# Optimization experiments

Hardware: AMD Instinct MI355X
Metric: run time of the kernel (lower is better)

Reference implementation:

```python
import jax, jax.numpy as jnp
import numpy as np

WIN_SIZE = 8          # img_size // win_num = 56 // 7
HEADS = 12
EMB = 384
HEAD_DIM = EMB // HEADS   # 32
ATT = WIN_SIZE ** 2       # 64 tokens per window
SCALE = HEAD_DIM ** -0.5
BATCH, NWIN = 32, 49


def _rel_index(ws: int) -> np.ndarray:
    # Faithful port of WinMSA.getIndex: relative-position index table (ws^2, ws^2)
    ys, xs = np.meshgrid(np.arange(ws), np.arange(ws), indexing='ij')
    coords = np.stack([ys, xs], axis=-1).reshape(-1, 2)            # (ws^2, 2)
    diff = coords[None, :, :] - coords[:, None, :] + (ws - 1)      # (ws^2, ws^2, 2)
    return diff[:, :, 0] * (2 * ws - 1) + diff[:, :, 1]            # values in [0, (2ws-1)^2)


def setup_inputs() -> dict:
    key = jax.random.key(0)
    k_x, k_qkv, k_pb, k_o = jax.random.split(key, 4)
    X = jax.random.normal(k_x, (BATCH, NWIN, ATT, EMB), dtype=jnp.float32)
    # qkv Linear (no bias): stored as (in, 3*in) so x @ W_qkv matches torch x @ W.T
    W_qkv = jax.random.normal(k_qkv, (EMB, 3 * EMB), dtype=jnp.float32) * 0.02
    # positional bias table, literal module shape (heads, 2*att-1, 2*att-1)
    pos_bias = jax.random.normal(k_pb, (HEADS, 2 * ATT - 1, 2 * ATT - 1), dtype=jnp.float32) * 0.02
    W_o = jax.random.normal(k_o, (EMB, EMB), dtype=jnp.float32) * 0.02
    b_o = jnp.zeros((EMB,), dtype=jnp.float32)
    relp = jnp.asarray(_rel_index(WIN_SIZE), dtype=jnp.int32)       # (ATT, ATT)
    return {"X": X, "W_qkv": W_qkv, "pos_bias": pos_bias, "W_o": W_o, "b_o": b_o, "relp": relp}


def reference(X, W_qkv, pos_bias, W_o, b_o, relp):
    B, Wn, S, E = X.shape
    # fused QKV projection
    qkv = (X @ W_qkv).reshape(B, Wn, S, 3, HEADS, HEAD_DIM)
    qkv = jnp.transpose(qkv, (3, 0, 1, 4, 2, 5))                    # (3, B, Wn, H, S, Dh)
    q, k, v = qkv[0], qkv[1], qkv[2]
    # gathered relative position bias: (H, S, S)
    bias = pos_bias.reshape(HEADS, -1)[:, relp]
    attn = jnp.einsum('bwhqd,bwhkd->bwhqk', q, k) * SCALE + bias[None, None]
    proba = jax.nn.softmax(attn, axis=-1)                           # dropout: eval mode (identity)
    out = jnp.einsum('bwhqk,bwhkd->bwhqd', proba, v)                # (B, Wn, H, S, Dh)
    out = jnp.transpose(out, (0, 1, 3, 2, 4)).reshape(B, Wn, S, E)
    return out @ W_o + b_o
```

## Files before the change

### kernel.cpp

```cpp
#include <hip/hip_runtime.h>
#include <hip/hip_bf16.h>

typedef float f32x4 __attribute__((ext_vector_type(4)));
typedef short s16x8 __attribute__((ext_vector_type(8)));

#define MFMA16(A,B,C) __builtin_amdgcn_mfma_f32_16x16x32_bf16((A),(B),(C),0,0,0)

__device__ __forceinline__ short f2bf(float f) {
  return (short)__bfloat16_as_ushort(__float2bfloat16(f));
}

__device__ __forceinline__ void gload_lds16(const void* g, void* l) {
  __builtin_amdgcn_global_load_lds(
      (const __attribute__((address_space(1))) unsigned*)g,
      (__attribute__((address_space(3))) unsigned*)l, 16, 0, 0);
}

__global__ __launch_bounds__(256) void prep_kernel(
    const float* __restrict__ Wqkv, const float* __restrict__ Wo,
    const float* __restrict__ posb, const int* __restrict__ relp,
    short* __restrict__ WqkvT, short* __restrict__ WoT, float* __restrict__ biasF)
{
  int i = blockIdx.x * 256 + threadIdx.x;
  if (i < 1152 * 384) {
    int n = i / 384, k = i % 384;
    WqkvT[i] = f2bf(Wqkv[k * 1152 + n]);
  } else if (i < 1152 * 384 + 384 * 384) {
    int j = i - 1152 * 384;
    int n = j / 384, k = j % 384;
    WoT[j] = f2bf(Wo[k * 384 + n]);
  } else {
    int j = i - (1152 * 384 + 384 * 384);
    int h = j >> 12, qk = j & 4095;
    biasF[j] = posb[h * 16129 + relp[qk]];
  }
}

__global__ __launch_bounds__(256) void xcvt_kernel(
    const float* __restrict__ X, short* __restrict__ Xbf)
{
  const int n8 = 4816896;
  for (int i = blockIdx.x * 256 + threadIdx.x; i < n8; i += gridDim.x * 256) {
    float4 a = *(const float4*)(X + (size_t)i * 8);
    float4 b = *(const float4*)(X + (size_t)i * 8 + 4);
    s16x8 p;
    p[0] = f2bf(a.x); p[1] = f2bf(a.y); p[2] = f2bf(a.z); p[3] = f2bf(a.w);
    p[4] = f2bf(b.x); p[5] = f2bf(b.y); p[6] = f2bf(b.z); p[7] = f2bf(b.w);
    *(s16x8*)(Xbf + (size_t)i * 8) = p;
  }
}

__global__ __launch_bounds__(256) void qkv_attn(
    const short* __restrict__ Xbf, const short* __restrict__ WqkvT,
    const float* __restrict__ biasF, short* __restrict__ AO)
{
  __shared__ short lds[40960];
  const int bid = blockIdx.x;
  const int wg = (bid & 7) * 588 + (bid >> 3);
  const int hg = wg % 6, mt = wg / 6;
  const int t = threadIdx.x;
  const int wv = t >> 6, l = t & 63, lr = l & 15, lg = l >> 4;
  const int wm = wv >> 1, wn = wv & 1;

  f32x4 acc[6][4];
#pragma unroll
  for (int fn = 0; fn < 6; ++fn)
#pragma unroll
    for (int fm = 0; fm < 4; ++fm) acc[fn][fm] = (f32x4)0.0f;

  const int cgs = (l & 7) ^ (l >> 3);
  const short* AbT = Xbf + (size_t)(mt * 128 + wv * 32 + (l >> 3)) * 384 + cgs * 8;
  const short* BbT[6];
#pragma unroll
  for (int j = 0; j < 6; ++j) {
    const int n0 = wv * 48 + j * 8 + (l >> 3);
    const int hl = n0 / 96, rem = n0 % 96;
    const int p = rem >> 5, d = rem & 31;
    BbT[j] = WqkvT + (size_t)(p * 384 + hg * 64 + hl * 32 + d) * 384 + cgs * 8;
  }

#define STAGE(KS, SEL) do {                                                  \
  _Pragma("unroll")                                                          \
  for (int i_ = 0; i_ < 4; ++i_)                                             \
    gload_lds16(AbT + i_ * 3072 + (KS) * 64,                                 \
                lds + (SEL) * 8192 + (wv * 4 + i_) * 512);                   \
  _Pragma("unroll")                                                          \
  for (int j_ = 0; j_ < 6; ++j_)                                             \
    gload_lds16(BbT[j_] + (KS) * 64,                                         \
                lds + 16384 + (SEL) * 12288 + (wv * 6 + j_) * 512);          \
  } while (0)

#define COMPUTE(SEL) do {                                                    \
  const short* Acur_ = lds + (SEL) * 8192;                                   \
  const short* Bcur_ = lds + 16384 + (SEL) * 12288;                          \
  _Pragma("unroll")                                                          \
  for (int kk = 0; kk < 2; ++kk) {                                           \
    s16x8 af[4], bq[6];                                                      \
    _Pragma("unroll")                                                        \
    for (int f = 0; f < 4; ++f) {                                            \
      const int arow = wm * 64 + f * 16 + lr;                                \
      const int ac = (kk * 4 + lg) ^ (arow & 7);                             \
      af[f] = *(const s16x8*)(Acur_ + arow * 64 + ac * 8);                   \
    }                                                                        \
    _Pragma("unroll")                                                        \
    for (int fn = 0; fn < 6; ++fn) {                                         \
      const int brow = wn * 96 + fn * 16 + lr;                               \
      const int bc = (kk * 4 + lg) ^ (brow & 7);                             \
      bq[fn] = *(const s16x8*)(Bcur_ + brow * 64 + bc * 8);                  \
    }                                                                        \
    _Pragma("unroll")                                                        \
    for (int fn = 0; fn < 6; ++fn)                                           \
      _Pragma("unroll")                                                      \
      for (int fm = 0; fm < 4; ++fm)                                         \
        acc[fn][fm] = MFMA16(bq[fn], af[fm], acc[fn][fm]);        \
  } } while (0)

#define ITER(T, WN) do {                                                     \
  asm volatile("s_waitcnt vmcnt(" #WN ")" ::: "memory");                     \
  __builtin_amdgcn_s_barrier();                                              \
  COMPUTE((T) & 1);                                                          \
  asm volatile("s_waitcnt lgkmcnt(0)" ::: "memory");          \
  __builtin_amdgcn_s_barrier();                                              \
  if ((T) + 2 < 6) STAGE((T) + 2, (T) & 1);                                  \
  } while (0)

  STAGE(0, 0);
  STAGE(1, 1);
  ITER(0, 10); ITER(1, 10); ITER(2, 10); ITER(3, 10); ITER(4, 10); ITER(5, 0);
#undef ITER
#undef COMPUTE
#undef STAGE


  const int w = mt * 2 + wm, h = hg * 2 + wn;
  short* Vts = lds + wv * 4992;
  short* Os  = Vts + 2432;

#pragma unroll
  for (int fv = 0; fv < 2; ++fv)
#pragma unroll
    for (int fm = 0; fm < 4; ++fm)
#pragma unroll
      for (int r = 0; r < 4; ++r)
        Vts[(fv * 16 + lg * 4 + r) * 76 + fm * 16 + lr] =
            f2bf(acc[4 + fv][fm][r]);

  s16x8 ka[4], qb[4];
#pragma unroll
  for (int f = 0; f < 4; ++f) {
    s16x8 tk, tq;
#pragma unroll
    for (int j = 0; j < 8; ++j) {
      tk[j] = f2bf(acc[2 + (j >> 2)][f][j & 3]);
      tq[j] = f2bf(acc[0 + (j >> 2)][f][j & 3]);
    }
    ka[f] = tk; qb[f] = tq;
  }

  f32x4 st[4][4];
#pragma unroll
  for (int fk = 0; fk < 4; ++fk)
#pragma unroll
    for (int fq = 0; fq < 4; ++fq)
      st[fk][fq] = MFMA16(ka[fk], qb[fq], (f32x4)0.0f);

  const float* bh = biasF + h * 4096;
#pragma unroll
  for (int fq = 0; fq < 4; ++fq) {
    const int q = fq * 16 + lr;
    float4 bv[4];
#pragma unroll
    for (int fk = 0; fk < 4; ++fk)
      bv[fk] = *(const float4*)(bh + q * 64 + fk * 16 + lg * 4);
    float mx = -3.0e38f;
#pragma unroll
    for (int fk = 0; fk < 4; ++fk)
#pragma unroll
      for (int r = 0; r < 4; ++r) {
        float v = st[fk][fq][r] * 0.17677669529663687f + ((const float*)&bv[fk])[r];
        st[fk][fq][r] = v;
        mx = fmaxf(mx, v);
      }
    mx = fmaxf(mx, __shfl_xor(mx, 16));
    mx = fmaxf(mx, __shfl_xor(mx, 32));
    float sm = 0.0f;
#pragma unroll
    for (int fk = 0; fk < 4; ++fk)
#pragma unroll
      for (int r = 0; r < 4; ++r) {
        float e = __expf(st[fk][fq][r] - mx);
        st[fk][fq][r] = e;
        sm += e;
      }
    sm += __shfl_xor(sm, 16);
    sm += __shfl_xor(sm, 32);
    const float inv = 1.0f / sm;
#pragma unroll
    for (int fk = 0; fk < 4; ++fk)
#pragma unroll
      for (int r = 0; r < 4; ++r) st[fk][fq][r] *= inv;
  }

  s16x8 va[2][2];
#pragma unroll
  for (int fd = 0; fd < 2; ++fd)
#pragma unroll
    for (int kb = 0; kb < 2; ++kb) {
      short4 v0 = *(const short4*)(Vts + (fd * 16 + lr) * 76 + kb * 32 + lg * 4);
      short4 v1 = *(const short4*)(Vts + (fd * 16 + lr) * 76 + kb * 32 + 16 + lg * 4);
      s16x8 tv;
      tv[0] = v0.x; tv[1] = v0.y; tv[2] = v0.z; tv[3] = v0.w;
      tv[4] = v1.x; tv[5] = v1.y; tv[6] = v1.z; tv[7] = v1.w;
      va[fd][kb] = tv;
    }
  f32x4 ot[2][4];
#pragma unroll
  for (int fd = 0; fd < 2; ++fd)
#pragma unroll
    for (int fq = 0; fq < 4; ++fq) ot[fd][fq] = (f32x4)0.0f;
#pragma unroll
  for (int kb = 0; kb < 2; ++kb)
#pragma unroll
    for (int fq = 0; fq < 4; ++fq) {
      s16x8 pb;
#pragma unroll
      for (int j = 0; j < 8; ++j)
        pb[j] = f2bf(st[2 * kb + (j >> 2)][fq][j & 3]);
#pragma unroll
      for (int fd = 0; fd < 2; ++fd)
        ot[fd][fq] = MFMA16(va[fd][kb], pb, ot[fd][fq]);
    }

#pragma unroll
  for (int fd = 0; fd < 2; ++fd)
#pragma unroll
    for (int fq = 0; fq < 4; ++fq)
#pragma unroll
      for (int r = 0; r < 4; ++r)
        Os[(fq * 16 + lr) * 40 + fd * 16 + lg * 4 + r] = f2bf(ot[fd][fq][r]);
  short* dst = AO + ((size_t)w * 64 + l) * 384 + h * 32;
  int4 o0 = *(const int4*)(Os + l * 40);
  int4 o1 = *(const int4*)(Os + l * 40 + 8);
  int4 o2 = *(const int4*)(Os + l * 40 + 16);
  int4 o3 = *(const int4*)(Os + l * 40 + 24);
  *(int4*)(dst)      = o0;
  *(int4*)(dst + 8)  = o1;
  *(int4*)(dst + 16) = o2;
  *(int4*)(dst + 24) = o3;
}

__global__ __launch_bounds__(256) void proj_kernel(
    const short* __restrict__ AO, const short* __restrict__ WoT,
    const float* __restrict__ bo, float* __restrict__ out)
{
  __shared__ short lds[32768];
  const int bid = blockIdx.x;
  const int wg = (bid & 7) * 294 + (bid >> 3);
  const int nt = wg % 3, mt = wg / 3;
  const int t = threadIdx.x;
  const int wv = t >> 6, l = t & 63, lr = l & 15, lg = l >> 4;
  const int wm = wv >> 1, wn = wv & 1;

  f32x4 acc[4][4];
#pragma unroll
  for (int fm = 0; fm < 4; ++fm)
#pragma unroll
    for (int fn = 0; fn < 4; ++fn) acc[fm][fn] = (f32x4)0.0f;

  const int srow = wv * 32 + (l >> 3);
  const int cg = (l & 7) ^ (srow & 7);
  const short* Ab = AO  + (size_t)(mt * 128 + srow) * 384 + cg * 8;
  const short* Bb = WoT + (size_t)(nt * 128 + srow) * 384 + cg * 8;

#define STAGE(KS, SEL) do {                                                  \
  _Pragma("unroll")                                                          \
  for (int i_ = 0; i_ < 4; ++i_) {                                           \
    gload_lds16(Ab + i_ * 3072 + (KS) * 64,                                  \
                lds + (SEL) * 16384 + (wv * 4 + i_) * 512);                  \
    gload_lds16(Bb + i_ * 3072 + (KS) * 64,                                  \
                lds + (SEL) * 16384 + 8192 + (wv * 4 + i_) * 512);           \
  } } while (0)

#define COMPUTE(SEL) do {                                                    \
  const short* Acur_ = lds + (SEL) * 16384;                                  \
  const short* Bcur_ = Acur_ + 8192;                                         \
  _Pragma("unroll")                                                          \
  for (int kk = 0; kk < 2; ++kk) {                                           \
    s16x8 af[4], bf[4];                                                      \
    _Pragma("unroll")                                                        \
    for (int f = 0; f < 4; ++f) {                                            \
      const int arow = wm * 64 + f * 16 + lr;                                \
      const int ac = (kk * 4 + lg) ^ (arow & 7);                             \
      af[f] = *(const s16x8*)(Acur_ + arow * 64 + ac * 8);                   \
      const int brow = wn * 64 + f * 16 + lr;                                \
      const int bc = (kk * 4 + lg) ^ (brow & 7);                             \
      bf[f] = *(const s16x8*)(Bcur_ + brow * 64 + bc * 8);                   \
    }                                                                        \
    _Pragma("unroll")                                                        \
    for (int fm = 0; fm < 4; ++fm)                                           \
      _Pragma("unroll")                                                      \
      for (int fn = 0; fn < 4; ++fn)                                         \
        acc[fm][fn] = MFMA16(af[fm], bf[fn], acc[fm][fn]);                   \
  } } while (0)

#define ITER(T, WN) do {                                                     \
  asm volatile("s_waitcnt vmcnt(" #WN ")" ::: "memory");                     \
  __builtin_amdgcn_s_barrier();                                              \
  COMPUTE((T) & 1);                                                          \
  asm volatile("s_waitcnt lgkmcnt(0)" ::: "memory");          \
  __builtin_amdgcn_s_barrier();                                              \
  if ((T) + 2 < 6) STAGE((T) + 2, (T) & 1);                                  \
  } while (0)

  STAGE(0, 0);
  STAGE(1, 1);
  ITER(0, 8); ITER(1, 8); ITER(2, 8); ITER(3, 8); ITER(4, 8); ITER(5, 0);
#undef ITER
#undef COMPUTE
#undef STAGE

#pragma unroll
  for (int fn = 0; fn < 4; ++fn) {
    const int n = nt * 128 + wn * 64 + fn * 16 + lr;
    const float bias = bo[n];
#pragma unroll
    for (int fm = 0; fm < 4; ++fm) {
      const int m0 = mt * 128 + wm * 64 + fm * 16 + lg * 4;
#pragma unroll
      for (int r = 0; r < 4; ++r)
        out[(size_t)(m0 + r) * 384 + n] = acc[fm][fn][r] + bias;
    }
  }
}

extern "C" void kernel_launch(void* const* d_in, const int* in_sizes, int n_in,
                              void* d_out, int out_size, void* d_ws, size_t ws_size,
                              hipStream_t stream)
{
  const float* X    = (const float*)d_in[0];
  const float* Wqkv = (const float*)d_in[1];
  const float* posb = (const float*)d_in[2];
  const float* Wo   = (const float*)d_in[3];
  const float* bo   = (const float*)d_in[4];
  const int*   relp = (const int*)d_in[5];
  float* out = (float*)d_out;

  char* ws = (char*)d_ws;
  short* WqkvT = (short*)(ws);
  short* WoT   = (short*)(ws + 884736);
  float* biasF = (float*)(ws + 1179648);
  short* Xbf   = (short*)(ws + 1376256);
  short* AO    = (short*)(ws + 78446592);

  prep_kernel<<<2496, 256, 0, stream>>>(Wqkv, Wo, posb, relp, WqkvT, WoT, biasF);
  xcvt_kernel<<<2048, 256, 0, stream>>>(X, Xbf);
  qkv_attn<<<4704, 256, 0, stream>>>(Xbf, WqkvT, biasF, AO);
  proj_kernel<<<2352, 256, 0, stream>>>(AO, WoT, bo, out);
}
```

Before: 232.6 us.

## Load QKV weight fragments directly into registers and shrink LDS for occupancy

The weight (B) operand of the QKV GEMM is no longer staged through LDS. Each wave now reads its MFMA fragments straight from global memory into registers inside the compute loop. The LDS allocation shrinks to just the X tiles and the attention scratch, and launch bounds request 4 blocks per CU so more workgroups can be resident. The trade-off is that the weight loads now sit in the vmcnt-ordered queue behind the prefetched A loads, so some global latency may be exposed instead of hidden by the double-buffered pipeline.

```diff
diff --git a/kernel.cpp b/kernel.cpp
--- a/kernel.cpp
+++ b/kernel.cpp
@@ -50,11 +50,11 @@
   }
 }
 
-__global__ __launch_bounds__(256) void qkv_attn(
+__global__ __launch_bounds__(256, 4) void qkv_attn(
     const short* __restrict__ Xbf, const short* __restrict__ WqkvT,
     const float* __restrict__ biasF, short* __restrict__ AO)
 {
-  __shared__ short lds[40960];
+  __shared__ short lds[19968];
   const int bid = blockIdx.x;
   const int wg = (bid & 7) * 588 + (bid >> 3);
   const int hg = wg % 6, mt = wg / 6;
@@ -70,32 +70,27 @@
 
   const int cgs = (l & 7) ^ (l >> 3);
   const short* AbT = Xbf + (size_t)(mt * 128 + wv * 32 + (l >> 3)) * 384 + cgs * 8;
-  const short* BbT[6];
-#pragma unroll
-  for (int j = 0; j < 6; ++j) {
-    const int n0 = wv * 48 + j * 8 + (l >> 3);
-    const int hl = n0 / 96, rem = n0 % 96;
-    const int p = rem >> 5, d = rem & 31;
-    BbT[j] = WqkvT + (size_t)(p * 384 + hg * 64 + hl * 32 + d) * 384 + cgs * 8;
-  }
+  const short* Bb[6];
+#pragma unroll
+  for (int fn = 0; fn < 6; ++fn)
+    Bb[fn] = WqkvT + (size_t)((fn >> 1) * 384 + hg * 64 + wn * 32
+                              + (fn & 1) * 16 + lr) * 384 + lg * 8;
 
 #define STAGE(KS, SEL) do {                                                  \
   _Pragma("unroll")                                                          \
   for (int i_ = 0; i_ < 4; ++i_)                                             \
     gload_lds16(AbT + i_ * 3072 + (KS) * 64,                                 \
                 lds + (SEL) * 8192 + (wv * 4 + i_) * 512);                   \
-  _Pragma("unroll")                                                          \
-  for (int j_ = 0; j_ < 6; ++j_)                                             \
-    gload_lds16(BbT[j_] + (KS) * 64,                                         \
-                lds + 16384 + (SEL) * 12288 + (wv * 6 + j_) * 512);          \
   } while (0)
 
-#define COMPUTE(SEL) do {                                                    \
-  const short* Acur_ = lds + (SEL) * 8192;                                   \
-  const short* Bcur_ = lds + 16384 + (SEL) * 12288;                          \
+#define COMPUTE(T) do {                                                      \
+  const short* Acur_ = lds + ((T) & 1) * 8192;                               \
   _Pragma("unroll")                                                          \
   for (int kk = 0; kk < 2; ++kk) {                                           \
     s16x8 af[4], bq[6];                                                      \
+    _Pragma("unroll")                                                        \
+    for (int fn = 0; fn < 6; ++fn)                                           \
+      bq[fn] = *(const s16x8*)(Bb[fn] + (T) * 64 + kk * 32);                 \
     _Pragma("unroll")                                                        \
     for (int f = 0; f < 4; ++f) {                                            \
       const int arow = wm * 64 + f * 16 + lr;                                \
@@ -103,12 +98,6 @@
       af[f] = *(const s16x8*)(Acur_ + arow * 64 + ac * 8);                   \
     }                                                                        \
     _Pragma("unroll")                                                        \
-    for (int fn = 0; fn < 6; ++fn) {                                         \
-      const int brow = wn * 96 + fn * 16 + lr;                               \
-      const int bc = (kk * 4 + lg) ^ (brow & 7);                             \
-      bq[fn] = *(const s16x8*)(Bcur_ + brow * 64 + bc * 8);                  \
-    }                                                                        \
-    _Pragma("unroll")                                                        \
     for (int fn = 0; fn < 6; ++fn)                                           \
       _Pragma("unroll")                                                      \
       for (int fm = 0; fm < 4; ++fm)                                         \
@@ -118,7 +107,7 @@
 #define ITER(T, WN) do {                                                     \
   asm volatile("s_waitcnt vmcnt(" #WN ")" ::: "memory");                     \
   __builtin_amdgcn_s_barrier();                                              \
-  COMPUTE((T) & 1);                                                          \
+  COMPUTE(T);                                                                \
   asm volatile("s_waitcnt lgkmcnt(0)" ::: "memory");          \
   __builtin_amdgcn_s_barrier();                                              \
   if ((T) + 2 < 6) STAGE((T) + 2, (T) & 1);                                  \
@@ -126,7 +115,7 @@
 
   STAGE(0, 0);
   STAGE(1, 1);
-  ITER(0, 10); ITER(1, 10); ITER(2, 10); ITER(3, 10); ITER(4, 10); ITER(5, 0);
+  ITER(0, 4); ITER(1, 4); ITER(2, 4); ITER(3, 4); ITER(4, 4); ITER(5, 0);
 #undef ITER
 #undef COMPUTE
 #undef STAGE
```

Result: slower. 863.0 us (+271.0%).

## Fuse X fp32-to-bf16 conversion into QKV attention kernel A-tile loads

Applied to the files above, without the earlier changes.

Removes the standalone conversion kernel and instead loads fp32 X tiles into registers inside the QKV/attention kernel, converting to bf16 and writing to LDS with software pipelining alongside the async weight loads. This eliminates a full write and reread of the bf16 copy of X and one kernel launch. In exchange, each block now reads twice as many bytes of X per tile, the tile is reread across head groups, and extra registers hold the prefetched fp32 data, which may reduce occupancy.

```diff
diff --git a/kernel.cpp b/kernel.cpp
--- a/kernel.cpp
+++ b/kernel.cpp
@@ -36,22 +36,8 @@
   }
 }
 
-__global__ __launch_bounds__(256) void xcvt_kernel(
-    const float* __restrict__ X, short* __restrict__ Xbf)
-{
-  const int n8 = 4816896;
-  for (int i = blockIdx.x * 256 + threadIdx.x; i < n8; i += gridDim.x * 256) {
-    float4 a = *(const float4*)(X + (size_t)i * 8);
-    float4 b = *(const float4*)(X + (size_t)i * 8 + 4);
-    s16x8 p;
-    p[0] = f2bf(a.x); p[1] = f2bf(a.y); p[2] = f2bf(a.z); p[3] = f2bf(a.w);
-    p[4] = f2bf(b.x); p[5] = f2bf(b.y); p[6] = f2bf(b.z); p[7] = f2bf(b.w);
-    *(s16x8*)(Xbf + (size_t)i * 8) = p;
-  }
-}
-
 __global__ __launch_bounds__(256) void qkv_attn(
-    const short* __restrict__ Xbf, const short* __restrict__ WqkvT,
+    const float* __restrict__ X, const short* __restrict__ WqkvT,
     const float* __restrict__ biasF, short* __restrict__ AO)
 {
   __shared__ short lds[40960];
@@ -69,7 +55,8 @@
     for (int fm = 0; fm < 4; ++fm) acc[fn][fm] = (f32x4)0.0f;
 
   const int cgs = (l & 7) ^ (l >> 3);
-  const short* AbT = Xbf + (size_t)(mt * 128 + wv * 32 + (l >> 3)) * 384 + cgs * 8;
+  const float* Axf = X + (size_t)(mt * 128 + wv * 32 + (l >> 3)) * 384 + cgs * 8;
+  const int adst = (wv * 32 + (l >> 3)) * 64 + (l & 7) * 8;
   const short* BbT[6];
 #pragma unroll
   for (int j = 0; j < 6; ++j) {
@@ -79,11 +66,28 @@
     BbT[j] = WqkvT + (size_t)(p * 384 + hg * 64 + hl * 32 + d) * 384 + cgs * 8;
   }
 
-#define STAGE(KS, SEL) do {                                                  \
-  _Pragma("unroll")                                                          \
-  for (int i_ = 0; i_ < 4; ++i_)                                             \
-    gload_lds16(AbT + i_ * 3072 + (KS) * 64,                                 \
-                lds + (SEL) * 8192 + (wv * 4 + i_) * 512);                   \
+  float4 a0[8], a1[8];
+
+#define ALOAD(SET, KS) do {                                                  \
+  _Pragma("unroll")                                                          \
+  for (int i_ = 0; i_ < 4; ++i_) {                                           \
+    const float* p_ = Axf + i_ * 8 * 384 + (KS) * 64;                        \
+    SET[2 * i_]     = *(const float4*)p_;                                    \
+    SET[2 * i_ + 1] = *(const float4*)(p_ + 4);                              \
+  } } while (0)
+
+#define AWRITE(SET, SEL) do {                                                \
+  _Pragma("unroll")                                                          \
+  for (int i_ = 0; i_ < 4; ++i_) {                                           \
+    s16x8 pk_;                                                               \
+    pk_[0] = f2bf(SET[2*i_].x);   pk_[1] = f2bf(SET[2*i_].y);                \
+    pk_[2] = f2bf(SET[2*i_].z);   pk_[3] = f2bf(SET[2*i_].w);                \
+    pk_[4] = f2bf(SET[2*i_+1].x); pk_[5] = f2bf(SET[2*i_+1].y);              \
+    pk_[6] = f2bf(SET[2*i_+1].z); pk_[7] = f2bf(SET[2*i_+1].w);              \
+    *(s16x8*)(lds + (SEL) * 8192 + adst + i_ * 512) = pk_;                   \
+  } } while (0)
+
+#define STAGE_B(KS, SEL) do {                                                \
   _Pragma("unroll")                                                          \
   for (int j_ = 0; j_ < 6; ++j_)                                             \
     gload_lds16(BbT[j_] + (KS) * 64,                                         \
@@ -115,21 +119,42 @@
         acc[fn][fm] = MFMA16(bq[fn], af[fm], acc[fn][fm]);        \
   } } while (0)
 
-#define ITER(T, WN) do {                                                     \
-  asm volatile("s_waitcnt vmcnt(" #WN ")" ::: "memory");                     \
+#define ITER(T, ACUR, ANXT, WTOP) do {                                       \
+  asm volatile("s_waitcnt vmcnt(" #WTOP ")" ::: "memory");                   \
   __builtin_amdgcn_s_barrier();                                              \
   COMPUTE((T) & 1);                                                          \
   asm volatile("s_waitcnt lgkmcnt(0)" ::: "memory");          \
   __builtin_amdgcn_s_barrier();                                              \
-  if ((T) + 2 < 6) STAGE((T) + 2, (T) & 1);                                  \
-  } while (0)
-
-  STAGE(0, 0);
-  STAGE(1, 1);
-  ITER(0, 10); ITER(1, 10); ITER(2, 10); ITER(3, 10); ITER(4, 10); ITER(5, 0);
+  if ((T) + 2 < 6) {                                                         \
+    STAGE_B((T) + 2, (T) & 1);                                               \
+    asm volatile("s_waitcnt vmcnt(6)" ::: "memory");      \
+    AWRITE(ACUR, (T) & 1);                                                   \
+    if ((T) + 3 < 6) ALOAD(ANXT, (T) + 3);                                   \
+    asm volatile("s_waitcnt lgkmcnt(0)" ::: "memory");   \
+  } } while (0)
+
+  ALOAD(a0, 0);
+  ALOAD(a1, 1);
+  STAGE_B(0, 0);
+  STAGE_B(1, 1);
+  asm volatile("s_waitcnt vmcnt(20)" ::: "memory");
+  AWRITE(a0, 0);
+  asm volatile("s_waitcnt vmcnt(12)" ::: "memory");
+  AWRITE(a1, 1);
+  ALOAD(a0, 2);
+  asm volatile("s_waitcnt lgkmcnt(0)" ::: "memory");
+
+  ITER(0, a0, a1, 14);
+  ITER(1, a1, a0, 14);
+  ITER(2, a0, a1, 14);
+  ITER(3, a1, a0, 14);
+  ITER(4, a0, a1, 6);
+  ITER(5, a1, a0, 0);
 #undef ITER
 #undef COMPUTE
-#undef STAGE
+#undef STAGE_B
+#undef AWRITE
+#undef ALOAD
 
 
   const int w = mt * 2 + wm, h = hg * 2 + wn;
@@ -349,11 +374,9 @@
   short* WqkvT = (short*)(ws);
   short* WoT   = (short*)(ws + 884736);
   float* biasF = (float*)(ws + 1179648);
-  short* Xbf   = (short*)(ws + 1376256);
-  short* AO    = (short*)(ws + 78446592);
+  short* AO    = (short*)(ws + 1376256);
 
   prep_kernel<<<2496, 256, 0, stream>>>(Wqkv, Wo, posb, relp, WqkvT, WoT, biasF);
-  xcvt_kernel<<<2048, 256, 0, stream>>>(X, Xbf);
-  qkv_attn<<<4704, 256, 0, stream>>>(Xbf, WqkvT, biasF, AO);
+  qkv_attn<<<4704, 256, 0, stream>>>(X, WqkvT, biasF, AO);
   proj_kernel<<<2352, 256, 0, stream>>>(AO, WoT, bo, out);
 }
```

Result: faster. 220.9 us (median of 2 runs) (-5.0%).
